# Optimization experiments

Hardware: AMD Instinct MI355X
Metric: run time of the kernel (lower is better)

## Reference

```python
import jax, jax.numpy as jnp
import numpy as np

B, C, H, W0, W1 = 2, 96, 64, 128, 128
NL, K, R = 2, 4, 6  # num_layers, cross-scan directions, dt_rank = ceil(C/16)
PNAMES = ['norm_w','norm_b','in_proj_w','conv_w','x_proj_w','dt_w','dt_b','A_logs','Ds',
          'out_norm_w','out_norm_b','out_proj_w','norm2_w','norm2_b','fc1_w','fc1_b','fc2_w','fc2_b']


def setup_inputs() -> dict:
    key = jax.random.key(0)
    ks = iter(jax.random.split(key, 40))
    def rn(shape, s=0.02):
        return jax.random.normal(next(ks), shape, jnp.float32) * s
    return dict(
        x0=jax.random.normal(next(ks), (B, C, H, W0), jnp.float32),
        x1=jax.random.normal(next(ks), (B, C, H, W1), jnp.float32),
        norm_w=jnp.ones((NL, C)), norm_b=jnp.zeros((NL, C)),
        in_proj_w=rn((NL, C, C)),                 # SS2D in_proj (Linear2d, bias=False)
        conv_w=rn((NL, C, 1, 3, 3), 0.1),         # depthwise 3x3, bias=False
        x_proj_w=rn((NL, K, R + 2, C)),           # dt_rank + 2*d_state rows (d_state=1)
        dt_w=rn((NL, K, C, R), 0.1),
        dt_b=rn((NL, K, C), 0.1),
        A_logs=jnp.zeros((NL, K, C)),             # v0 init with d_state=1 -> log(1)=0
        Ds=jnp.ones((NL, K, C)),
        out_norm_w=jnp.ones((NL, C)), out_norm_b=jnp.zeros((NL, C)),
        out_proj_w=rn((NL, C, C)),                # bias=False
        norm2_w=jnp.ones((NL, C)), norm2_b=jnp.zeros((NL, C)),
        fc1_w=rn((NL, 4 * C, C)), fc1_b=jnp.zeros((NL, 4 * C)),
        fc2_w=rn((NL, C, 4 * C)), fc2_b=jnp.zeros((NL, C)),
    )


def ln2d(x, w, b, eps=1e-5):
    # LayerNorm2d: normalize over channel dim of NCHW
    mu = x.mean(1, keepdims=True)
    var = ((x - mu) ** 2).mean(1, keepdims=True)
    return (x - mu) * jax.lax.rsqrt(var + eps) * w[None, :, None, None] + b[None, :, None, None]


def conv1x1(x, w):  # Linear2d: w (out,in)
    return jnp.einsum('bchw,dc->bdhw', x, w)


def dwconv3(x, w):  # depthwise 3x3, SAME padding
    return jax.lax.conv_general_dilated(x, w, (1, 1), 'SAME',
        dimension_numbers=('NCHW', 'OIHW', 'NCHW'), feature_group_count=x.shape[1])


def linear_scan(a, b):
    # h_t = a_t * h_{t-1} + b_t along last axis, via associative scan
    def comb(l, r):
        al, bl = l
        ar, br = r
        return (ar * al, ar * bl + br)
    return jax.lax.associative_scan(comb, (a, b), axis=-1)[1]


def ss2d(x, p):
    # SS2Dv2 forward_type='v05_noz', channel_first, d_state=1
    Bs_, Cd, Hh, Ww = x.shape
    Ll = Hh * Ww
    x = conv1x1(x, p['in_proj_w'])
    x = jax.nn.silu(dwconv3(x, p['conv_w']))
    # CrossScan: row-major, col-major, and their flips -> (B,K,C,L)
    xs0 = x.reshape(Bs_, Cd, Ll)
    xs1 = x.transpose(0, 1, 3, 2).reshape(Bs_, Cd, Ll)
    xs = jnp.stack([xs0, xs1, xs0[..., ::-1], xs1[..., ::-1]], 1)
    xdbl = jnp.einsum('bkcl,kdc->bkdl', xs, p['x_proj_w'])
    dts, Bmat, Cmat = xdbl[:, :, :R], xdbl[:, :, R:R + 1], xdbl[:, :, R + 1:R + 2]
    delta = jax.nn.softplus(jnp.einsum('bkrl,kcr->bkcl', dts, p['dt_w']) + p['dt_b'][None, :, :, None])
    A = -jnp.exp(p['A_logs'])                       # (K,C), scalar state
    a = jnp.exp(delta * A[None, :, :, None])        # (B,K,C,L)
    bterm = delta * Bmat * xs                       # Bmat broadcasts over C (d_state=1)
    h = linear_scan(a, bterm)
    ys = Cmat * h + p['Ds'][None, :, :, None] * xs  # (B,K,C,L)
    # CrossMerge: un-flip dirs 2,3; map col-major back to row-major; sum
    y_row = ys[:, 0] + ys[:, 2, :, ::-1]
    y_col = ys[:, 1] + ys[:, 3, :, ::-1]
    y_col = y_col.reshape(Bs_, Cd, Ww, Hh).transpose(0, 1, 3, 2).reshape(Bs_, Cd, Ll)
    y = (y_row + y_col).reshape(Bs_, Cd, Hh, Ww)
    y = ln2d(y, p['out_norm_w'], p['out_norm_b'])
    return conv1x1(y, p['out_proj_w'])


def block(x, p):
    # drop_path is identity in eval mode; all dropout rates are 0
    x = x + ss2d(ln2d(x, p['norm_w'], p['norm_b']), p)
    h = conv1x1(ln2d(x, p['norm2_w'], p['norm2_b']), p['fc1_w']) + p['fc1_b'][None, :, None, None]
    h = jax.nn.gelu(h, approximate=False)
    return x + conv1x1(h, p['fc2_w']) + p['fc2_b'][None, :, None, None]


def run_stack(x, params):
    for i in range(NL):
        p = {k: v[i] for k, v in params.items()}
        x = block(x, p)
    return x


def _forward(x0, x1, params):
    x = jnp.concatenate([x0, x1], -1)
    xb = x[..., ::-1]
    x = run_stack(x, params)
    xb = run_stack(xb, params)
    xbf = xb[..., ::-1]
    w0 = x0.shape[-1]
    y0 = 0.5 * (x[..., :w0] + xbf[..., :w0])
    y1 = 0.5 * (x[..., w0:] + xbf[..., w0:])
    return (y0, y1)


def reference(x0, x1, norm_w, norm_b, in_proj_w, conv_w, x_proj_w, dt_w, dt_b, A_logs, Ds,
              out_norm_w, out_norm_b, out_proj_w, norm2_w, norm2_b, fc1_w, fc1_b, fc2_w, fc2_b):
    params = dict(zip(PNAMES, [norm_w, norm_b, in_proj_w, conv_w, x_proj_w, dt_w, dt_b, A_logs, Ds,
                               out_norm_w, out_norm_b, out_proj_w, norm2_w, norm2_b, fc1_w, fc1_b, fc2_w, fc2_b]))
    return _forward(x0, x1, params)
```

## Files before the change

### kernel.cpp

```cpp
#include <hip/hip_runtime.h>
#include <cstdint>
#include <cstddef>

#define BT 4
#define CC 96
#define HH 64
#define WW 256
#define LL (HH*WW)
#define KD 4
#define RR 6
#define NLAY 2
#define C4 (4*CC)
#define SLOTF 47424
#define STPW 4096
#define WARM 512

typedef unsigned short u16;
typedef __attribute__((ext_vector_type(8))) short bf16x8;
typedef __attribute__((ext_vector_type(4))) float f32x4;

__device__ __forceinline__ u16 f2bf(float f){
  unsigned u = __float_as_uint(f);
  unsigned r = (u + 0x7FFFu + ((u >> 16) & 1u)) >> 16;
  return (u16)r;
}
__device__ __forceinline__ float bf2f(u16 h){
  return __uint_as_float(((unsigned)h) << 16);
}
__device__ __forceinline__ unsigned pk_bf16(float lo, float hi){
  unsigned r;
  asm volatile("v_cvt_pk_bf16_f32 %0, %1, %2" : "=v"(r) : "v"(lo), "v"(hi));
  return r;
}
__device__ __forceinline__ float fexp2(float x){
  float r; asm("v_exp_f32 %0, %1" : "=v"(r) : "v"(x)); return r;
}
__device__ __forceinline__ float flog2(float x){
  float r; asm("v_log_f32 %0, %1" : "=v"(r) : "v"(x)); return r;
}
__device__ __forceinline__ float gelu_f(float v){
  float t = v*v;
  float u = v*fmaf(0.0356774081f, t, 0.7978845608f);
  float e2 = __expf(2.f*u);
  float r = __builtin_amdgcn_rcpf(e2 + 1.f);
  return fmaf(-v, r, v);
}

__global__ void k_build(const float* __restrict__ x0, const float* __restrict__ x1,
                        float* __restrict__ X){
  size_t i = (size_t)blockIdx.x*256 + threadIdx.x;
  size_t tot = (size_t)2*CC*HH*WW;
  if (i >= tot) return;
  int w = i % WW; size_t r = i / WW;
  int h = r % HH; size_t bc = r / HH;
  float val;
  if (w < 128) val = x0[(bc*HH + h)*128 + w];
  else         val = x1[(bc*HH + h)*128 + (w-128)];
  X[i] = val;
  size_t ib = ((bc + (size_t)2*CC)*HH + h)*WW + (WW-1-w);
  X[ib] = val;
}

template<bool ST, typename T>
__global__ __launch_bounds__(256) void k_pack(const T* __restrict__ src,
      u16* __restrict__ dst, float* __restrict__ st){
  __shared__ float tl[CC][33];
  int tid = threadIdx.x;
  int l0 = blockIdx.x*32, b = blockIdx.y;
  for (int e = tid; e < CC*32; e += 256){
    int c = e >> 5, dl = e & 31;
    T raw = src[((size_t)b*CC + c)*LL + l0 + dl];
    float vv;
    if constexpr (sizeof(T) == 2) vv = bf2f((u16)raw); else vv = (float)raw;
    tl[c][dl] = vv;
  }
  __syncthreads();
  if (ST && tid < 32){
    float s = 0.f, ss = 0.f;
    for (int c = 0; c < CC; ++c){ float vv = tl[c][tid]; s += vv; ss += vv*vv; }
    float mu = s*(1.f/CC);
    float var = ss*(1.f/CC) - mu*mu;
    st[(size_t)b*LL + l0 + tid] = mu;
    st[(size_t)BT*LL + (size_t)b*LL + l0 + tid] = rsqrtf(var + 1e-5f);
  }
  int dl = tid >> 3, cg = tid & 7;
  u16* dp = dst + ((size_t)b*LL + l0 + dl)*104 + cg*12;
  #pragma unroll
  for (int q = 0; q < 3; ++q){
    ushort4 pk;
    pk.x = f2bf(tl[cg*12 + q*4 + 0][dl]);
    pk.y = f2bf(tl[cg*12 + q*4 + 1][dl]);
    pk.z = f2bf(tl[cg*12 + q*4 + 2][dl]);
    pk.w = f2bf(tl[cg*12 + q*4 + 3][dl]);
    *(ushort4*)(dp + q*4) = pk;
  }
}

template<int M, int K, bool FC1ORD, bool LNF, bool BIAS>
__global__ void k_prepw(const float* __restrict__ W, const float* __restrict__ lnw,
      const float* __restrict__ lnb, const float* __restrict__ bias,
      u16* __restrict__ Wb, float* __restrict__ s1, float* __restrict__ cadd){
  int lay = blockIdx.y;
  W += (size_t)lay*M*K;
  Wb += (size_t)lay*SLOTF*2;
  s1 += (size_t)lay*SLOTF;
  cadd += (size_t)lay*SLOTF;
  int m = blockIdx.x*64 + threadIdx.x;
  if (m >= M) return;
  int rowfrag = m >> 4, lr = m & 15;
  float s1v = 0.f, sbv = 0.f;
  for (int c = 0; c < K; ++c){
    float wv = W[(size_t)m*K + c];
    float wf = LNF ? wv*lnw[lay*K + c] : wv;
    u16 h = f2bf(wf);
    int colfrag = c >> 5, lg = (c >> 3) & 3, j = c & 7;
    int f;
    if (FC1ORD) f = (rowfrag/6)*18 + colfrag*6 + (rowfrag % 6);
    else        f = colfrag*(M/16) + rowfrag;
    Wb[(size_t)(f*64 + lg*16 + lr)*8 + j] = h;
    s1v += bf2f(h);
    if (LNF) sbv = fmaf(wv, lnb[lay*K + c], sbv);
  }
  if (BIAS) sbv += bias[lay*M + m];
  s1[m] = s1v;
  cadd[m] = sbv;
}

template<bool LNF, bool RES, bool WF32, bool WBF, bool STATS, bool WPB>
__global__ __launch_bounds__(256) void k_gmm2(
    const u16* __restrict__ Wb, const u16* __restrict__ inT,
    float* __restrict__ outF, u16* __restrict__ outT,
    const float* __restrict__ s1v, const float* __restrict__ cadd,
    const float* __restrict__ res,
    const float* __restrict__ stI, float* __restrict__ stO,
    u16* __restrict__ outPB){
  __shared__ u16 bt[128*104];
  int tid = threadIdx.x, lane = tid & 63, wid = tid >> 6;
  int l0 = blockIdx.x*128;
  int lr = lane & 15, lg = lane >> 4;
  const int4* bsrc = (const int4*)(inT + (size_t)l0*104);
  for (int i = tid; i < 1664; i += 256) ((int4*)bt)[i] = bsrc[i];
  __syncthreads();
  f32x4 acc[6][2];
  #pragma unroll
  for (int mf = 0; mf < 6; ++mf){ acc[mf][0] = (f32x4){0,0,0,0}; acc[mf][1] = (f32x4){0,0,0,0}; }
  #pragma unroll
  for (int ks = 0; ks < 3; ++ks){
    bf16x8 af[6];
    #pragma unroll
    for (int mf = 0; mf < 6; ++mf)
      af[mf] = *(const bf16x8*)(Wb + (size_t)((ks*6 + mf)*64 + lane)*8);
    bf16x8 bfr[2];
    #pragma unroll
    for (int ls = 0; ls < 2; ++ls)
      bfr[ls] = *(const bf16x8*)&bt[(wid*32 + ls*16 + lr)*104 + ks*32 + lg*8];
    #pragma unroll
    for (int mf = 0; mf < 6; ++mf)
      #pragma unroll
      for (int ls = 0; ls < 2; ++ls)
        acc[mf][ls] = __builtin_amdgcn_mfma_f32_16x16x32_bf16(af[mf], bfr[ls], acc[mf][ls], 0, 0, 0);
  }
  #pragma unroll
  for (int ls = 0; ls < 2; ++ls){
    int l = l0 + wid*32 + ls*16 + lr;
    int b = l >> 14, lb = l & (LL-1);
    float mu = 0.f, rs = 0.f;
    if (LNF){ mu = stI[l]; rs = stI[(size_t)BT*LL + l]; }
    float ssum = 0.f, ssq = 0.f;
    #pragma unroll
    for (int mf = 0; mf < 6; ++mf){
      float o[4];
      #pragma unroll
      for (int r = 0; r < 4; ++r){
        int mm = mf*16 + lg*4 + r;
        float vv = acc[mf][ls][r];
        if (LNF) vv = fmaf(rs, vv, fmaf(-mu*rs, s1v[mm], cadd[mm]));
        else     vv += cadd[mm];
        if (RES) vv += res[((size_t)b*96 + mm)*LL + lb];
        if (WF32) outF[((size_t)b*96 + mm)*LL + lb] = vv;
        if (WPB)  outPB[((size_t)b*96 + mm)*LL + lb] = f2bf(vv);
        if (STATS){ ssum += vv; ssq += vv*vv; }
        o[r] = vv;
      }
      if (WBF){
        ushort4 pk;
        pk.x = f2bf(o[0]); pk.y = f2bf(o[1]); pk.z = f2bf(o[2]); pk.w = f2bf(o[3]);
        *(ushort4*)(outT + (size_t)l*104 + mf*16 + lg*4) = pk;
      }
    }
    if (STATS){
      ssum += __shfl_xor(ssum, 16); ssq += __shfl_xor(ssq, 16);
      ssum += __shfl_xor(ssum, 32); ssq += __shfl_xor(ssq, 32);
      if (lane < 16){
        float mu2 = ssum*(1.f/CC);
        float var = ssq*(1.f/CC) - mu2*mu2;
        stO[l] = mu2;
        stO[(size_t)BT*LL + l] = rsqrtf(var + 1e-5f);
      }
    }
  }
}

__global__ __launch_bounds__(512, 4) void k_mlp(
    const u16* __restrict__ Wb1, const u16* __restrict__ Wb2,
    const u16* __restrict__ XT, float* __restrict__ X, u16* __restrict__ XTout,
    const float* __restrict__ s11, const float* __restrict__ c1,
    const float* __restrict__ c2,
    const float* __restrict__ stI, float* __restrict__ stO){
  __shared__ u16 bt[128*104];
  __shared__ u16 hs[128*104];
  int tid = threadIdx.x, lane = tid & 63, wid = tid >> 6;
  int l0 = blockIdx.x*128;
  int lr = lane & 15, lg = lane >> 4;
  const int4* bsrc = (const int4*)(XT + (size_t)l0*104);
  for (int i = tid; i < 1664; i += 512) ((int4*)bt)[i] = bsrc[i];

  int l = l0 + wid*16 + lr;
  float mu = stI[l];
  float rs = stI[(size_t)BT*LL + l];
  float nmr = -mu*rs;
  __syncthreads();

  int hrow = (wid*16 + lr)*104;
  f32x4 acc2[6];
  #pragma unroll
  for (int mf = 0; mf < 6; ++mf) acc2[mf] = (f32x4){0,0,0,0};

  for (int cc = 0; cc < 4; ++cc){
    f32x4 acc1[6];
    #pragma unroll
    for (int mf = 0; mf < 6; ++mf) acc1[mf] = (f32x4){0,0,0,0};
    #pragma unroll
    for (int ks = 0; ks < 3; ++ks){
      bf16x8 af[6];
      #pragma unroll
      for (int mf = 0; mf < 6; ++mf)
        af[mf] = *(const bf16x8*)(Wb1 + (size_t)((cc*18 + ks*6 + mf)*64 + lane)*8);
      bf16x8 bfr = *(const bf16x8*)&bt[hrow + ks*32 + lg*8];
      #pragma unroll
      for (int mf = 0; mf < 6; ++mf)
        acc1[mf] = __builtin_amdgcn_mfma_f32_16x16x32_bf16(af[mf], bfr, acc1[mf], 0, 0, 0);
    }
    #pragma unroll
    for (int mf = 0; mf < 6; ++mf){
      float4 sv = *(const float4*)&s11[cc*96 + mf*16 + lg*4];
      float4 cv = *(const float4*)&c1 [cc*96 + mf*16 + lg*4];
      float g0 = gelu_f(fmaf(rs, acc1[mf][0], fmaf(nmr, sv.x, cv.x)));
      float g1 = gelu_f(fmaf(rs, acc1[mf][1], fmaf(nmr, sv.y, cv.y)));
      float g2 = gelu_f(fmaf(rs, acc1[mf][2], fmaf(nmr, sv.z, cv.z)));
      float g3 = gelu_f(fmaf(rs, acc1[mf][3], fmaf(nmr, sv.w, cv.w)));
      uint2 pw;
      pw.x = pk_bf16(g0, g1);
      pw.y = pk_bf16(g2, g3);
      *(uint2*)&hs[hrow + mf*16 + lg*4] = pw;
    }
    #pragma unroll
    for (int ks = 0; ks < 3; ++ks){
      bf16x8 a2[6];
      #pragma unroll
      for (int mf2 = 0; mf2 < 6; ++mf2)
        a2[mf2] = *(const bf16x8*)(Wb2 + (size_t)(((cc*3 + ks)*6 + mf2)*64 + lane)*8);
      bf16x8 bfr2 = *(const bf16x8*)&hs[hrow + ks*32 + lg*8];
      #pragma unroll
      for (int mf2 = 0; mf2 < 6; ++mf2)
        acc2[mf2] = __builtin_amdgcn_mfma_f32_16x16x32_bf16(a2[mf2], bfr2, acc2[mf2], 0, 0, 0);
    }
  }
  {
    int b = l >> 14, lb = l & (LL-1);
    float ssum = 0.f, ssq = 0.f;
    #pragma unroll
    for (int mf = 0; mf < 6; ++mf){
      float o[4];
      #pragma unroll
      for (int r = 0; r < 4; ++r){
        int mm = mf*16 + lg*4 + r;
        float vv = acc2[mf][r] + c2[mm];
        vv += X[((size_t)b*96 + mm)*LL + lb];
        X[((size_t)b*96 + mm)*LL + lb] = vv;
        ssum += vv; ssq += vv*vv;
        o[r] = vv;
      }
      ushort4 pk;
      pk.x = f2bf(o[0]); pk.y = f2bf(o[1]); pk.z = f2bf(o[2]); pk.w = f2bf(o[3]);
      *(ushort4*)(XTout + (size_t)l*104 + mf*16 + lg*4) = pk;
    }
    ssum += __shfl_xor(ssum, 16); ssq += __shfl_xor(ssq, 16);
    ssum += __shfl_xor(ssum, 32); ssq += __shfl_xor(ssq, 32);
    if (lane < 16){
      float mu2 = ssum*(1.f/CC);
      float var = ssq*(1.f/CC) - mu2*mu2;
      stO[l] = mu2;
      stO[(size_t)BT*LL + l] = rsqrtf(var + 1e-5f);
    }
  }
}

__global__ __launch_bounds__(256) void k_dwconv_silu_t(const u16* __restrict__ u,
      u16* __restrict__ v, u16* __restrict__ vT, const float* __restrict__ cw){
  __shared__ float tl[32][33];
  int bc = blockIdx.z;
  int c = bc % CC;
  int w0 = blockIdx.x*32, h0 = blockIdx.y*32;
  const u16* up = u + (size_t)bc*LL;
  const float* k9 = cw + c*9;
  int t = threadIdx.x;
  int wl = (t & 7)*4, hl = t >> 3;
  int h = h0 + hl, w = w0 + wl;
  float acc[4] = {0.f,0.f,0.f,0.f};
  #pragma unroll
  for (int dh = -1; dh <= 1; ++dh){
    int h2 = h + dh;
    if (h2 < 0 || h2 >= HH) continue;
    const u16* row = up + (size_t)h2*WW + w;
    ushort4 mq = *(const ushort4*)row;
    float m0 = bf2f(mq.x), m1 = bf2f(mq.y), m2 = bf2f(mq.z), m3 = bf2f(mq.w);
    float lft = (w > 0) ? bf2f(row[-1]) : 0.f;
    float rgt = (w + 4 < WW) ? bf2f(row[4]) : 0.f;
    float k0 = k9[(dh+1)*3], k1 = k9[(dh+1)*3+1], k2 = k9[(dh+1)*3+2];
    acc[0] += lft*k0 + m0*k1 + m1*k2;
    acc[1] += m0*k0 + m1*k1 + m2*k2;
    acc[2] += m1*k0 + m2*k1 + m3*k2;
    acc[3] += m2*k0 + m3*k1 + rgt*k2;
  }
  float s[4];
  #pragma unroll
  for (int j = 0; j < 4; ++j){
    float a = acc[j];
    float e = __expf(-a);
    s[j] = a * __builtin_amdgcn_rcpf(1.f + e);
    tl[wl + j][hl] = s[j];
  }
  uint2 pw;
  pw.x = pk_bf16(s[0], s[1]);
  pw.y = pk_bf16(s[2], s[3]);
  *(uint2*)&v[(size_t)bc*LL + (size_t)h*WW + w] = pw;
  __syncthreads();
  int ww = t >> 3, hh4 = (t & 7)*4;
  uint2 po;
  po.x = pk_bf16(tl[ww][hh4],   tl[ww][hh4+1]);
  po.y = pk_bf16(tl[ww][hh4+2], tl[ww][hh4+3]);
  *(uint2*)&vT[(size_t)bc*LL + (size_t)(w0 + ww)*HH + h0 + hh4] = po;
}

__global__ void k_xproj(const u16* __restrict__ v, const u16* __restrict__ vT,
                        u16* __restrict__ G, const float* __restrict__ xpw){
  int which = blockIdx.y;
  const u16* src = which ? vT : v;
  int kA = which ? 1 : 0, kB = which ? 3 : 2;
  size_t i = (size_t)blockIdx.x*256 + threadIdx.x;
  if (i >= (size_t)BT*LL) return;
  int b = (int)(i / LL), l = (int)(i % LL);
  const u16* sp = src + (size_t)b*CC*LL + l;
  const float* wA = xpw + (size_t)kA*8*CC;
  const float* wB = xpw + (size_t)kB*8*CC;
  float aA[8], aB[8];
  #pragma unroll
  for (int d = 0; d < 8; ++d){ aA[d] = 0.f; aB[d] = 0.f; }
  for (int c = 0; c < CC; ++c){
    float xv = bf2f(sp[(size_t)c*LL]);
    #pragma unroll
    for (int d = 0; d < 8; ++d){
      aA[d] = fmaf(wA[d*CC + c], xv, aA[d]);
      aB[d] = fmaf(wB[d*CC + c], xv, aB[d]);
    }
  }
  u16* gA = G + (((size_t)b*KD + kA)*8)*LL + l;
  u16* gB = G + (((size_t)b*KD + kB)*8)*LL + l;
  #pragma unroll
  for (int d = 0; d < 8; ++d){ gA[(size_t)d*LL] = f2bf(aA[d]); gB[(size_t)d*LL] = f2bf(aB[d]); }
}

__device__ __forceinline__ void ldbf8(const u16* p, float* o){
  uint4 t = *(const uint4*)p;
  o[0]=bf2f((u16)(t.x & 0xffff)); o[1]=bf2f((u16)(t.x >> 16));
  o[2]=bf2f((u16)(t.y & 0xffff)); o[3]=bf2f((u16)(t.y >> 16));
  o[4]=bf2f((u16)(t.z & 0xffff)); o[5]=bf2f((u16)(t.z >> 16));
  o[6]=bf2f((u16)(t.w & 0xffff)); o[7]=bf2f((u16)(t.w >> 16));
}
__device__ __forceinline__ void rev8(float* a){
  #pragma unroll
  for (int i = 0; i < 4; ++i){ float t0 = a[i]; a[i] = a[7-i]; a[7-i] = t0; }
}

__global__ __launch_bounds__(256) void k_scan3(const u16* __restrict__ G,
                       const u16* __restrict__ v, const u16* __restrict__ vT,
                       u16* __restrict__ Y,
                       const float* __restrict__ dtw_, const float* __restrict__ dtb_,
                       const float* __restrict__ Alog_, const float* __restrict__ Ds_){
  const size_t SZ = (size_t)BT*CC*LL;
  const float LOG2E = 1.4426950408889634f, LN2 = 0.6931471805599453f;
  int wid = threadIdx.x >> 6, lane = threadIdx.x & 63;
  int tile = wid;
  int sy = blockIdx.y;
  bool rev = (blockIdx.z != 0);
  int c = sy % CC; int t2 = sy / CC; int kk = t2 & 1; int b = t2 >> 1;
  int k = (rev ? 2 : 0) + kk;
  const u16* src = (kk ? vT : v) + ((size_t)b*CC + c)*LL;
  const u16* g = G + (((size_t)b*KD + k)*8)*LL;
  float dtw[RR];
  #pragma unroll
  for (int r = 0; r < RR; ++r) dtw[r] = dtw_[((size_t)k*CC + c)*RR + r];
  float dtb = dtb_[k*CC + c];
  float A  = -__expf(Alog_[k*CC + c]);
  float Dv = Ds_[k*CC + c];
  u16* yout = Y + (size_t)k*SZ + ((size_t)b*CC + c)*LL;

  int lstore0 = tile*STPW;
  float carry = 0.f;
  for (int p = 0; p < 1 + STPW/WARM; ++p){
    int base = lstore0 - WARM + p*WARM;
    if (base < 0) continue;
    bool st = (base >= lstore0);
    int l = base + (lane<<3);
    int ga = rev ? (LL-8-l) : l;
    float dsum[8], g6b[8], g7b[8], xb[8];
    #pragma unroll
    for (int i = 0; i < 8; ++i) dsum[i] = dtb;
    #pragma unroll
    for (int r = 0; r < RR; ++r){
      float t8[8];
      ldbf8(g + (size_t)r*LL + ga, t8);
      #pragma unroll
      for (int i = 0; i < 8; ++i) dsum[i] = fmaf(t8[i], dtw[r], dsum[i]);
    }
    ldbf8(g + (size_t)6*LL + ga, g6b);
    if (st){
      ldbf8(g + (size_t)7*LL + ga, g7b);
    } else {
      #pragma unroll
      for (int i = 0; i < 8; ++i) g7b[i] = 0.f;
    }
    ldbf8(src + ga, xb);
    if (rev){ rev8(dsum); rev8(g6b); rev8(g7b); rev8(xb); }
    float av[8], bt[8];
    #pragma unroll
    for (int i = 0; i < 8; ++i){
      float dl2 = dsum[i]*LOG2E;
      float y = flog2(1.f + fexp2(dl2));
      y = (dsum[i] > 20.f) ? dl2 : y;
      float delta = y*LN2;
      av[i] = fexp2(A*y);
      bt[i] = delta * g6b[i] * xb[i];
    }
    float P = av[0], Q = bt[0];
    #pragma unroll
    for (int i = 1; i < 8; ++i){ Q = fmaf(av[i], Q, bt[i]); P *= av[i]; }
    #pragma unroll
    for (int off = 1; off < 64; off <<= 1){
      float Pp = __shfl_up(P, (unsigned)off);
      float Qp = __shfl_up(Q, (unsigned)off);
      if (lane >= off){ Q = fmaf(P, Qp, Q); P *= Pp; }
    }
    float Pe = __shfl_up(P, 1u), Qe = __shfl_up(Q, 1u);
    if (lane == 0){ Pe = 1.f; Qe = 0.f; }
    float h = fmaf(Pe, carry, Qe);
    if (st){
      float ys[8];
      #pragma unroll
      for (int i = 0; i < 8; ++i){
        h = fmaf(av[i], h, bt[i]);
        ys[i] = fmaf(g7b[i], h, Dv*xb[i]);
      }
      carry = __shfl(h, 63);
      if (rev) rev8(ys);
      uint4 pw;
      pw.x = pk_bf16(ys[0], ys[1]);
      pw.y = pk_bf16(ys[2], ys[3]);
      pw.z = pk_bf16(ys[4], ys[5]);
      pw.w = pk_bf16(ys[6], ys[7]);
      *(uint4*)&yout[ga] = pw;
    } else {
      #pragma unroll
      for (int i = 0; i < 8; ++i) h = fmaf(av[i], h, bt[i]);
      carry = __shfl(h, 63);
    }
  }
}

__global__ __launch_bounds__(256) void k_combine4(const u16* __restrict__ Y, u16* __restrict__ z){
  const size_t SZ = (size_t)BT*CC*LL;
  __shared__ float tl[64][65];
  int bc = blockIdx.z;
  int w0 = blockIdx.x*64;
  int t = threadIdx.x;
  const u16* y1p = Y + SZ   + (size_t)bc*LL;
  const u16* y3p = Y + 3*SZ + (size_t)bc*LL;
  {
    int wl = t >> 2;
    int h0 = (t & 3)*16;
    size_t base = (size_t)(w0 + wl)*HH + h0;
    #pragma unroll
    for (int j = 0; j < 4; ++j){
      ushort4 a = *(const ushort4*)&y1p[base + j*4];
      ushort4 bq = *(const ushort4*)&y3p[base + j*4];
      tl[wl][h0 + j*4 + 0] = bf2f(a.x) + bf2f(bq.x);
      tl[wl][h0 + j*4 + 1] = bf2f(a.y) + bf2f(bq.y);
      tl[wl][h0 + j*4 + 2] = bf2f(a.z) + bf2f(bq.z);
      tl[wl][h0 + j*4 + 3] = bf2f(a.w) + bf2f(bq.w);
    }
  }
  __syncthreads();
  const u16* y0p = Y +        (size_t)bc*LL;
  const u16* y2p = Y + 2*SZ + (size_t)bc*LL;
  u16* zp = z + (size_t)bc*LL;
  {
    int h = t >> 2;
    int wq = (t & 3)*16;
    #pragma unroll
    for (int j = 0; j < 4; ++j){
      int wl = wq + j*4;
      size_t idx = (size_t)h*WW + w0 + wl;
      ushort4 a = *(const ushort4*)&y0p[idx];
      ushort4 bq = *(const ushort4*)&y2p[idx];
      ushort4 o;
      o.x = f2bf(bf2f(a.x) + bf2f(bq.x) + tl[wl+0][h]);
      o.y = f2bf(bf2f(a.y) + bf2f(bq.y) + tl[wl+1][h]);
      o.z = f2bf(bf2f(a.z) + bf2f(bq.z) + tl[wl+2][h]);
      o.w = f2bf(bf2f(a.w) + bf2f(bq.w) + tl[wl+3][h]);
      *(ushort4*)&zp[idx] = o;
    }
  }
}

__global__ void k_output(const float* __restrict__ X, float* __restrict__ out){
  size_t i = (size_t)blockIdx.x*256 + threadIdx.x;
  size_t half = (size_t)2*CC*HH*128;
  if (i >= half) return;
  int w = i % 128; size_t r = i / 128;
  int h = r % HH; size_t bc = r / HH;
  size_t fwd = (bc*HH + h)*WW;
  size_t bwd = ((bc + (size_t)2*CC)*HH + h)*WW;
  out[i]        = 0.5f*(X[fwd + w]       + X[bwd + (WW-1-w)]);
  out[half + i] = 0.5f*(X[fwd + 128 + w] + X[bwd + (127 - w)]);
}

extern "C" void kernel_launch(void* const* d_in, const int* in_sizes, int n_in,
                              void* d_out, int out_size, void* d_ws, size_t ws_size,
                              hipStream_t stream){
  const float* x0        = (const float*)d_in[0];
  const float* x1        = (const float*)d_in[1];
  const float* norm_w    = (const float*)d_in[2];
  const float* norm_b    = (const float*)d_in[3];
  const float* in_proj_w = (const float*)d_in[4];
  const float* conv_w    = (const float*)d_in[5];
  const float* x_proj_w  = (const float*)d_in[6];
  const float* dt_w      = (const float*)d_in[7];
  const float* dt_b      = (const float*)d_in[8];
  const float* A_logs    = (const float*)d_in[9];
  const float* Ds        = (const float*)d_in[10];
  const float* out_norm_w= (const float*)d_in[11];
  const float* out_norm_b= (const float*)d_in[12];
  const float* out_proj_w= (const float*)d_in[13];
  const float* norm2_w   = (const float*)d_in[14];
  const float* norm2_b   = (const float*)d_in[15];
  const float* fc1_w     = (const float*)d_in[16];
  const float* fc1_b     = (const float*)d_in[17];
  const float* fc2_w     = (const float*)d_in[18];
  const float* fc2_b     = (const float*)d_in[19];

  const size_t SZ = (size_t)BT*CC*LL;
  float* X  = (float*)d_ws;
  float* t  = X + SZ;
  float* u  = t + SZ;
  float* G  = u + SZ;
  float* v  = G + (size_t)BT*KD*8*LL;
  float* vT = v + SZ;
  float* Yf = vT + SZ;
  u16*   Gb = (u16*)G;
  u16*   Yb = (u16*)Yf;
  u16*   XT = (u16*)Yf;
  u16*   uB = (u16*)u;
  u16*   vB = (u16*)v;
  u16*   vTB= (u16*)vT;
  u16*   tB = (u16*)t;
  u16*   tT = (u16*)u;
  float* ext = Yf + 4*SZ;
  float* stats_X = ext;
  float* stats_t = stats_X + 2*(size_t)BT*LL;
  float* wsl     = stats_t + 2*(size_t)BT*LL;

  float* p0 = wsl;
  u16*  WbI0 = (u16*)p0;          float* s1I0 = p0 + 4608;  float* cI0 = p0 + 4704;
  u16*  WbO0 = (u16*)(p0+4800);   float* s1O0 = p0 + 9408;  float* cO0 = p0 + 9504;
  u16*  Wb10 = (u16*)(p0+9600);   float* s110 = p0 + 28032; float* c10 = p0 + 28416;
  u16*  Wb20 = (u16*)(p0+28800);  float* s120 = p0 + 47232; float* c20 = p0 + 47328;

  k_prepw<96,96,false,true,false><<<dim3(2,NLAY),64,0,stream>>>(in_proj_w, norm_w, norm_b, nullptr, WbI0, s1I0, cI0);
  k_prepw<96,96,false,true,false><<<dim3(2,NLAY),64,0,stream>>>(out_proj_w, out_norm_w, out_norm_b, nullptr, WbO0, s1O0, cO0);
  k_prepw<384,96,true,true,true><<<dim3(6,NLAY),64,0,stream>>>(fc1_w, norm2_w, norm2_b, fc1_b, Wb10, s110, c10);
  k_prepw<96,384,false,false,true><<<dim3(2,NLAY),64,0,stream>>>(fc2_w, nullptr, nullptr, fc2_b, Wb20, s120, c20);

  k_build<<<(2*CC*HH*WW + 255)/256, 256, 0, stream>>>(x0, x1, X);
  k_pack<true,float><<<dim3(LL/32, BT), 256, 0, stream>>>(X, XT, stats_X);

  for (int lay = 0; lay < NLAY; ++lay){
    size_t so = (size_t)lay*SLOTF;
    const u16* WbI = WbI0 + so*2; const float* s1I = s1I0 + so; const float* cI = cI0 + so;
    const u16* WbO = WbO0 + so*2; const float* s1O = s1O0 + so; const float* cO = cO0 + so;
    const u16* Wb1 = Wb10 + so*2; const float* s11 = s110 + so; const float* c1 = c10 + so;
    const u16* Wb2 = Wb20 + so*2; const float* c2 = c20 + so;
    const float* cw  = conv_w    + (size_t)lay*CC*9;
    const float* xpw = x_proj_w  + (size_t)lay*KD*8*CC;
    const float* dw  = dt_w      + (size_t)lay*KD*CC*RR;
    const float* db  = dt_b      + (size_t)lay*KD*CC;
    const float* Al  = A_logs    + (size_t)lay*KD*CC;
    const float* Dp  = Ds        + (size_t)lay*KD*CC;

    k_gmm2<true,false,false,false,false,true><<<dim3(BT*LL/128),256,0,stream>>>(
        WbI, XT, nullptr, nullptr, s1I, cI, nullptr, stats_X, nullptr, uB);
    k_dwconv_silu_t<<<dim3(8,2,BT*CC), 256, 0, stream>>>(uB, vB, vTB, cw);
    k_xproj<<<dim3(BT*LL/256, 2), 256, 0, stream>>>(vB, vTB, Gb, xpw);
    k_scan3<<<dim3(1,768,2), 256, 0, stream>>>(Gb, vB, vTB, Yb, dw, db, Al, Dp);
    k_combine4<<<dim3(4,1,BT*CC), 256, 0, stream>>>(Yb, tB);
    k_pack<true,u16><<<dim3(LL/32, BT), 256, 0, stream>>>(tB, tT, stats_t);
    k_gmm2<true,true,true,true,true,false><<<dim3(BT*LL/128),256,0,stream>>>(
        WbO, tT, X, XT, s1O, cO, X, stats_t, stats_X, nullptr);
    k_mlp<<<dim3(BT*LL/128),512,0,stream>>>(
        Wb1, Wb2, XT, X, XT, s11, c1, c2, stats_X, stats_X);
  }

  k_output<<<(unsigned)(((size_t)2*CC*HH*128 + 255)/256), 256, 0, stream>>>(X, (float*)d_out);
}
```

Baseline: 403.4 us.

## Keep residual stream in bf16 and fuse transpose/LN stats into projection kernels

```diff
diff --git a/kernel.cpp b/kernel.cpp
--- a/kernel.cpp
+++ b/kernel.cpp
@@ -47,7 +47,7 @@
 }
 
 __global__ void k_build(const float* __restrict__ x0, const float* __restrict__ x1,
-                        float* __restrict__ X){
+                        u16* __restrict__ X){
   size_t i = (size_t)blockIdx.x*256 + threadIdx.x;
   size_t tot = (size_t)2*CC*HH*WW;
   if (i >= tot) return;
@@ -56,44 +56,10 @@
   float val;
   if (w < 128) val = x0[(bc*HH + h)*128 + w];
   else         val = x1[(bc*HH + h)*128 + (w-128)];
-  X[i] = val;
+  u16 hv = f2bf(val);
+  X[i] = hv;
   size_t ib = ((bc + (size_t)2*CC)*HH + h)*WW + (WW-1-w);
-  X[ib] = val;
-}
-
-template<bool ST, typename T>
-__global__ __launch_bounds__(256) void k_pack(const T* __restrict__ src,
-      u16* __restrict__ dst, float* __restrict__ st){
-  __shared__ float tl[CC][33];
-  int tid = threadIdx.x;
-  int l0 = blockIdx.x*32, b = blockIdx.y;
-  for (int e = tid; e < CC*32; e += 256){
-    int c = e >> 5, dl = e & 31;
-    T raw = src[((size_t)b*CC + c)*LL + l0 + dl];
-    float vv;
-    if constexpr (sizeof(T) == 2) vv = bf2f((u16)raw); else vv = (float)raw;
-    tl[c][dl] = vv;
-  }
-  __syncthreads();
-  if (ST && tid < 32){
-    float s = 0.f, ss = 0.f;
-    for (int c = 0; c < CC; ++c){ float vv = tl[c][tid]; s += vv; ss += vv*vv; }
-    float mu = s*(1.f/CC);
-    float var = ss*(1.f/CC) - mu*mu;
-    st[(size_t)b*LL + l0 + tid] = mu;
-    st[(size_t)BT*LL + (size_t)b*LL + l0 + tid] = rsqrtf(var + 1e-5f);
-  }
-  int dl = tid >> 3, cg = tid & 7;
-  u16* dp = dst + ((size_t)b*LL + l0 + dl)*104 + cg*12;
-  #pragma unroll
-  for (int q = 0; q < 3; ++q){
-    ushort4 pk;
-    pk.x = f2bf(tl[cg*12 + q*4 + 0][dl]);
-    pk.y = f2bf(tl[cg*12 + q*4 + 1][dl]);
-    pk.z = f2bf(tl[cg*12 + q*4 + 2][dl]);
-    pk.w = f2bf(tl[cg*12 + q*4 + 3][dl]);
-    *(ushort4*)(dp + q*4) = pk;
-  }
+  X[ib] = hv;
 }
 
 template<int M, int K, bool FC1ORD, bool LNF, bool BIAS>
@@ -126,21 +92,48 @@
   cadd[m] = sbv;
 }
 
-template<bool LNF, bool RES, bool WF32, bool WBF, bool STATS, bool WPB>
-__global__ __launch_bounds__(256) void k_gmm2(
-    const u16* __restrict__ Wb, const u16* __restrict__ inT,
-    float* __restrict__ outF, u16* __restrict__ outT,
-    const float* __restrict__ s1v, const float* __restrict__ cadd,
-    const float* __restrict__ res,
-    const float* __restrict__ stI, float* __restrict__ stO,
-    u16* __restrict__ outPB){
+template<bool RES>
+__global__ __launch_bounds__(256) void k_proj(
+    const u16* __restrict__ Wb, const u16* __restrict__ inP,
+    u16* __restrict__ outP, const u16* __restrict__ resP,
+    const float* __restrict__ s1v, const float* __restrict__ cadd){
   __shared__ u16 bt[128*104];
+  __shared__ float sA[2][128], sB[2][128], sm[128], sr[128];
   int tid = threadIdx.x, lane = tid & 63, wid = tid >> 6;
   int l0 = blockIdx.x*128;
+  int b = l0 >> 14, lb0 = l0 & (LL-1);
   int lr = lane & 15, lg = lane >> 4;
-  const int4* bsrc = (const int4*)(inT + (size_t)l0*104);
-  for (int i = tid; i < 1664; i += 256) ((int4*)bt)[i] = bsrc[i];
+  {
+    int px = tid & 127, grp = tid >> 7;
+    int ch0 = grp*48;
+    const u16* ip = inP + ((size_t)b*CC + ch0)*LL + lb0 + px;
+    u16 ch[48];
+    float s = 0.f, ss = 0.f;
+    #pragma unroll
+    for (int j = 0; j < 48; ++j){
+      ch[j] = ip[(size_t)j*LL];
+      float xv = bf2f(ch[j]);
+      s += xv; ss += xv*xv;
+    }
+    #pragma unroll
+    for (int j2 = 0; j2 < 12; ++j2){
+      uint2 w2;
+      w2.x = (unsigned)ch[j2*4+0] | ((unsigned)ch[j2*4+1] << 16);
+      w2.y = (unsigned)ch[j2*4+2] | ((unsigned)ch[j2*4+3] << 16);
+      *(uint2*)&bt[px*104 + ch0 + j2*4] = w2;
+    }
+    sA[grp][px] = s;
+    sB[grp][px] = ss;
+  }
   __syncthreads();
+  if (tid < 128){
+    float s = sA[0][tid] + sA[1][tid];
+    float ss = sB[0][tid] + sB[1][tid];
+    float mu = s*(1.f/CC);
+    float var = ss*(1.f/CC) - mu*mu;
+    sm[tid] = mu;
+    sr[tid] = rsqrtf(var + 1e-5f);
+  }
   f32x4 acc[6][2];
   #pragma unroll
   for (int mf = 0; mf < 6; ++mf){ acc[mf][0] = (f32x4){0,0,0,0}; acc[mf][1] = (f32x4){0,0,0,0}; }
@@ -160,42 +153,21 @@
       for (int ls = 0; ls < 2; ++ls)
         acc[mf][ls] = __builtin_amdgcn_mfma_f32_16x16x32_bf16(af[mf], bfr[ls], acc[mf][ls], 0, 0, 0);
   }
+  __syncthreads();
   #pragma unroll
   for (int ls = 0; ls < 2; ++ls){
-    int l = l0 + wid*32 + ls*16 + lr;
-    int b = l >> 14, lb = l & (LL-1);
-    float mu = 0.f, rs = 0.f;
-    if (LNF){ mu = stI[l]; rs = stI[(size_t)BT*LL + l]; }
-    float ssum = 0.f, ssq = 0.f;
+    int row = wid*32 + ls*16 + lr;
+    float mu = sm[row], rs = sr[row];
+    float nmr = -mu*rs;
     #pragma unroll
     for (int mf = 0; mf < 6; ++mf){
-      float o[4];
       #pragma unroll
       for (int r = 0; r < 4; ++r){
         int mm = mf*16 + lg*4 + r;
-        float vv = acc[mf][ls][r];
-        if (LNF) vv = fmaf(rs, vv, fmaf(-mu*rs, s1v[mm], cadd[mm]));
-        else     vv += cadd[mm];
-        if (RES) vv += res[((size_t)b*96 + mm)*LL + lb];
-        if (WF32) outF[((size_t)b*96 + mm)*LL + lb] = vv;
-        if (WPB)  outPB[((size_t)b*96 + mm)*LL + lb] = f2bf(vv);
-        if (STATS){ ssum += vv; ssq += vv*vv; }
-        o[r] = vv;
-      }
-      if (WBF){
-        ushort4 pk;
-        pk.x = f2bf(o[0]); pk.y = f2bf(o[1]); pk.z = f2bf(o[2]); pk.w = f2bf(o[3]);
-        *(ushort4*)(outT + (size_t)l*104 + mf*16 + lg*4) = pk;
-      }
-    }
-    if (STATS){
-      ssum += __shfl_xor(ssum, 16); ssq += __shfl_xor(ssq, 16);
-      ssum += __shfl_xor(ssum, 32); ssq += __shfl_xor(ssq, 32);
-      if (lane < 16){
-        float mu2 = ssum*(1.f/CC);
-        float var = ssq*(1.f/CC) - mu2*mu2;
-        stO[l] = mu2;
-        stO[(size_t)BT*LL + l] = rsqrtf(var + 1e-5f);
+        float vv = fmaf(rs, acc[mf][ls][r], fmaf(nmr, s1v[mm], cadd[mm]));
+        size_t idx = ((size_t)b*CC + mm)*LL + lb0 + row;
+        if (RES) vv += bf2f(resP[idx]);
+        outP[idx] = f2bf(vv);
       }
     }
   }
@@ -203,25 +175,55 @@
 
 __global__ __launch_bounds__(512, 4) void k_mlp(
     const u16* __restrict__ Wb1, const u16* __restrict__ Wb2,
-    const u16* __restrict__ XT, float* __restrict__ X, u16* __restrict__ XTout,
+    u16* __restrict__ X,
     const float* __restrict__ s11, const float* __restrict__ c1,
-    const float* __restrict__ c2,
-    const float* __restrict__ stI, float* __restrict__ stO){
+    const float* __restrict__ c2){
   __shared__ u16 bt[128*104];
   __shared__ u16 hs[128*104];
+  __shared__ float sm[128], sr[128];
+  float* sA = (float*)hs;
+  float* sB = sA + 512;
   int tid = threadIdx.x, lane = tid & 63, wid = tid >> 6;
   int l0 = blockIdx.x*128;
+  int b = l0 >> 14, lb0 = l0 & (LL-1);
   int lr = lane & 15, lg = lane >> 4;
-  const int4* bsrc = (const int4*)(XT + (size_t)l0*104);
-  for (int i = tid; i < 1664; i += 512) ((int4*)bt)[i] = bsrc[i];
-
-  int l = l0 + wid*16 + lr;
-  float mu = stI[l];
-  float rs = stI[(size_t)BT*LL + l];
-  float nmr = -mu*rs;
+  {
+    int px = tid & 127, grp = tid >> 7;
+    int ch0 = grp*24;
+    const u16* ip = X + ((size_t)b*CC + ch0)*LL + lb0 + px;
+    u16 ch[24];
+    float s = 0.f, ss = 0.f;
+    #pragma unroll
+    for (int j = 0; j < 24; ++j){
+      ch[j] = ip[(size_t)j*LL];
+      float xv = bf2f(ch[j]);
+      s += xv; ss += xv*xv;
+    }
+    #pragma unroll
+    for (int j2 = 0; j2 < 6; ++j2){
+      uint2 w2;
+      w2.x = (unsigned)ch[j2*4+0] | ((unsigned)ch[j2*4+1] << 16);
+      w2.y = (unsigned)ch[j2*4+2] | ((unsigned)ch[j2*4+3] << 16);
+      *(uint2*)&bt[px*104 + ch0 + j2*4] = w2;
+    }
+    sA[grp*128 + px] = s;
+    sB[grp*128 + px] = ss;
+  }
   __syncthreads();
-
-  int hrow = (wid*16 + lr)*104;
+  if (tid < 128){
+    float s = sA[tid] + sA[128+tid] + sA[256+tid] + sA[384+tid];
+    float ss = sB[tid] + sB[128+tid] + sB[256+tid] + sB[384+tid];
+    float mu = s*(1.f/CC);
+    float var = ss*(1.f/CC) - mu*mu;
+    sm[tid] = mu;
+    sr[tid] = rsqrtf(var + 1e-5f);
+  }
+  __syncthreads();
+  int row = wid*16 + lr;
+  float rs = sr[row];
+  float nmr = -sm[row]*rs;
+
+  int hrow = row*104;
   f32x4 acc2[6];
   #pragma unroll
   for (int mf = 0; mf < 6; ++mf) acc2[mf] = (f32x4){0,0,0,0};
@@ -266,32 +268,14 @@
         acc2[mf2] = __builtin_amdgcn_mfma_f32_16x16x32_bf16(a2[mf2], bfr2, acc2[mf2], 0, 0, 0);
     }
   }
-  {
-    int b = l >> 14, lb = l & (LL-1);
-    float ssum = 0.f, ssq = 0.f;
-    #pragma unroll
-    for (int mf = 0; mf < 6; ++mf){
-      float o[4];
-      #pragma unroll
-      for (int r = 0; r < 4; ++r){
-        int mm = mf*16 + lg*4 + r;
-        float vv = acc2[mf][r] + c2[mm];
-        vv += X[((size_t)b*96 + mm)*LL + lb];
-        X[((size_t)b*96 + mm)*LL + lb] = vv;
-        ssum += vv; ssq += vv*vv;
-        o[r] = vv;
-      }
-      ushort4 pk;
-      pk.x = f2bf(o[0]); pk.y = f2bf(o[1]); pk.z = f2bf(o[2]); pk.w = f2bf(o[3]);
-      *(ushort4*)(XTout + (size_t)l*104 + mf*16 + lg*4) = pk;
-    }
-    ssum += __shfl_xor(ssum, 16); ssq += __shfl_xor(ssq, 16);
-    ssum += __shfl_xor(ssum, 32); ssq += __shfl_xor(ssq, 32);
-    if (lane < 16){
-      float mu2 = ssum*(1.f/CC);
-      float var = ssq*(1.f/CC) - mu2*mu2;
-      stO[l] = mu2;
-      stO[(size_t)BT*LL + l] = rsqrtf(var + 1e-5f);
+  #pragma unroll
+  for (int mf = 0; mf < 6; ++mf){
+    #pragma unroll
+    for (int r = 0; r < 4; ++r){
+      int mm = mf*16 + lg*4 + r;
+      size_t idx = ((size_t)b*CC + mm)*LL + lb0 + row;
+      float vv = acc2[mf][r] + c2[mm] + bf2f(X[idx]);
+      X[idx] = f2bf(vv);
     }
   }
 }
@@ -523,7 +507,7 @@
   }
 }
 
-__global__ void k_output(const float* __restrict__ X, float* __restrict__ out){
+__global__ void k_output(const u16* __restrict__ X, float* __restrict__ out){
   size_t i = (size_t)blockIdx.x*256 + threadIdx.x;
   size_t half = (size_t)2*CC*HH*128;
   if (i >= half) return;
@@ -531,8 +515,8 @@
   int h = r % HH; size_t bc = r / HH;
   size_t fwd = (bc*HH + h)*WW;
   size_t bwd = ((bc + (size_t)2*CC)*HH + h)*WW;
-  out[i]        = 0.5f*(X[fwd + w]       + X[bwd + (WW-1-w)]);
-  out[half + i] = 0.5f*(X[fwd + 128 + w] + X[bwd + (127 - w)]);
+  out[i]        = 0.5f*(bf2f(X[fwd + w])       + bf2f(X[bwd + (WW-1-w)]));
+  out[half + i] = 0.5f*(bf2f(X[fwd + 128 + w]) + bf2f(X[bwd + (127 - w)]));
 }
 
 extern "C" void kernel_launch(void* const* d_in, const int* in_sizes, int n_in,
@@ -560,25 +544,14 @@
   const float* fc2_b     = (const float*)d_in[19];
 
   const size_t SZ = (size_t)BT*CC*LL;
-  float* X  = (float*)d_ws;
-  float* t  = X + SZ;
-  float* u  = t + SZ;
-  float* G  = u + SZ;
-  float* v  = G + (size_t)BT*KD*8*LL;
-  float* vT = v + SZ;
-  float* Yf = vT + SZ;
-  u16*   Gb = (u16*)G;
-  u16*   Yb = (u16*)Yf;
-  u16*   XT = (u16*)Yf;
-  u16*   uB = (u16*)u;
-  u16*   vB = (u16*)v;
-  u16*   vTB= (u16*)vT;
-  u16*   tB = (u16*)t;
-  u16*   tT = (u16*)u;
-  float* ext = Yf + 4*SZ;
-  float* stats_X = ext;
-  float* stats_t = stats_X + 2*(size_t)BT*LL;
-  float* wsl     = stats_t + 2*(size_t)BT*LL;
+  u16* Xb  = (u16*)d_ws;
+  u16* tB  = Xb + SZ;
+  u16* uB  = tB + SZ;
+  u16* vB  = uB + SZ;
+  u16* vTB = vB + SZ;
+  u16* Gb  = vTB + SZ;
+  u16* Yb  = Gb + (size_t)BT*KD*8*LL;
+  float* wsl = (float*)(Yb + 4*SZ);
 
   float* p0 = wsl;
   u16*  WbI0 = (u16*)p0;          float* s1I0 = p0 + 4608;  float* cI0 = p0 + 4704;
@@ -591,8 +564,7 @@
   k_prepw<384,96,true,true,true><<<dim3(6,NLAY),64,0,stream>>>(fc1_w, norm2_w, norm2_b, fc1_b, Wb10, s110, c10);
   k_prepw<96,384,false,false,true><<<dim3(2,NLAY),64,0,stream>>>(fc2_w, nullptr, nullptr, fc2_b, Wb20, s120, c20);
 
-  k_build<<<(2*CC*HH*WW + 255)/256, 256, 0, stream>>>(x0, x1, X);
-  k_pack<true,float><<<dim3(LL/32, BT), 256, 0, stream>>>(X, XT, stats_X);
+  k_build<<<(2*CC*HH*WW + 255)/256, 256, 0, stream>>>(x0, x1, Xb);
 
   for (int lay = 0; lay < NLAY; ++lay){
     size_t so = (size_t)lay*SLOTF;
@@ -607,18 +579,14 @@
     const float* Al  = A_logs    + (size_t)lay*KD*CC;
     const float* Dp  = Ds        + (size_t)lay*KD*CC;
 
-    k_gmm2<true,false,false,false,false,true><<<dim3(BT*LL/128),256,0,stream>>>(
-        WbI, XT, nullptr, nullptr, s1I, cI, nullptr, stats_X, nullptr, uB);
+    k_proj<false><<<dim3(BT*LL/128),256,0,stream>>>(WbI, Xb, uB, nullptr, s1I, cI);
     k_dwconv_silu_t<<<dim3(8,2,BT*CC), 256, 0, stream>>>(uB, vB, vTB, cw);
     k_xproj<<<dim3(BT*LL/256, 2), 256, 0, stream>>>(vB, vTB, Gb, xpw);
     k_scan3<<<dim3(1,768,2), 256, 0, stream>>>(Gb, vB, vTB, Yb, dw, db, Al, Dp);
     k_combine4<<<dim3(4,1,BT*CC), 256, 0, stream>>>(Yb, tB);
-    k_pack<true,u16><<<dim3(LL/32, BT), 256, 0, stream>>>(tB, tT, stats_t);
-    k_gmm2<true,true,true,true,true,false><<<dim3(BT*LL/128),256,0,stream>>>(
-        WbO, tT, X, XT, s1O, cO, X, stats_t, stats_X, nullptr);
-    k_mlp<<<dim3(BT*LL/128),512,0,stream>>>(
-        Wb1, Wb2, XT, X, XT, s11, c1, c2, stats_X, stats_X);
-  }
-
-  k_output<<<(unsigned)(((size_t)2*CC*HH*128 + 255)/256), 256, 0, stream>>>(X, (float*)d_out);
-}
+    k_proj<true><<<dim3(BT*LL/128),256,0,stream>>>(WbO, tB, Xb, Xb, s1O, cO);
+    k_mlp<<<dim3(BT*LL/128),512,0,stream>>>(Wb1, Wb2, Xb, s11, c1, c2);
+  }
+
+  k_output<<<(unsigned)(((size_t)2*CC*HH*128 + 255)/256), 256, 0, stream>>>(Xb, (float*)d_out);
+}
```

After: 360.1 us. -10.7%, faster.
